# Kernel tuning notes

Measured on AMD Instinct MI355X. Metric: run time of the kernel, lower is better.

Reference implementation:

```python
import jax, jax.numpy as jnp
import numpy as np

T = 32768
H = 1024
N_HARM = 100
N_NOISE = 65
N_MLP = 3
LN_EPS = 1e-6

def exp_sigmoid(x, exponent=10.0, max_value=2.0, threshold=1e-7):
    return max_value * jax.nn.sigmoid(x) ** jnp.log(exponent) + threshold

def setup_inputs() -> dict:
    key = jax.random.key(0)
    ks = jax.random.split(key, 16)
    g = lambda k, shape, fan_in: jax.random.normal(k, shape, jnp.float32) / np.sqrt(fan_in)
    return {
        "f0": jax.random.uniform(ks[0], (T,), jnp.float32),
        "loudness": jax.random.normal(ks[1], (T,), jnp.float32),
        "W_in": g(ks[2], (2, H), 2), "b_in": jnp.zeros((H,), jnp.float32),
        "Wi": g(ks[3], (H, 3 * H), H),      # input kernels [r|z|n], no bias
        "Wh": g(ks[4], (H, 3 * H), H),      # hidden kernels [r|z|n]
        "b_h": jnp.zeros((3 * H,), jnp.float32),
        "h0": jnp.zeros((H,), jnp.float32),
        "mlp_W": g(ks[5], (N_MLP, H, H), H), "mlp_b": jnp.zeros((N_MLP, H), jnp.float32),
        "ln_scale": jnp.ones((N_MLP, H), jnp.float32), "ln_bias": jnp.zeros((N_MLP, H), jnp.float32),
        "amp_W": g(ks[6], (H, 1), H), "amp_b": jnp.zeros((1,), jnp.float32),
        "harm_W": g(ks[7], (H, N_HARM), H), "harm_b": jnp.zeros((N_HARM,), jnp.float32),
        "noise_W": g(ks[8], (H, N_NOISE), H), "noise_b": jnp.full((N_NOISE,), -5.0, jnp.float32),
    }

def _layernorm(x, scale, bias):
    mu = jnp.mean(x, axis=-1, keepdims=True)
    var = jnp.mean(jnp.square(x - mu), axis=-1, keepdims=True)
    return (x - mu) * jax.lax.rsqrt(var + LN_EPS) * scale + bias

def reference(f0, loudness, W_in, b_in, Wi, Wh, b_h, h0, mlp_W, mlp_b, ln_scale, ln_bias,
              amp_W, amp_b, harm_W, harm_b, noise_W, noise_b):
    features = jnp.stack([f0, loudness], axis=-1)          # [T, 2]
    projected = features @ W_in + b_in                     # [T, H]
    # Precompute input-side gate projections for all timesteps (one big GEMM).
    gi_all = projected @ Wi                                # [T, 3H]

    def gru_step(h, gi):
        gh = h @ Wh + b_h                                  # [3H]
        gi_r, gi_z, gi_n = jnp.split(gi, 3)
        gh_r, gh_z, gh_n = jnp.split(gh, 3)
        r = jax.nn.sigmoid(gi_r + gh_r)
        z = jax.nn.sigmoid(gi_z + gh_z)
        n = jnp.tanh(gi_n + r * gh_n)
        h_new = (1.0 - z) * n + z * h
        return h_new, h_new

    _, h = jax.lax.scan(gru_step, h0, gi_all)              # [T, H]
    for i in range(N_MLP):
        h = jax.nn.relu(_layernorm(h @ mlp_W[i] + mlp_b[i], ln_scale[i], ln_bias[i]))
    overall_amp = exp_sigmoid(h @ amp_W + amp_b)           # [T, 1]
    harmonic_dist = exp_sigmoid(h @ harm_W + harm_b)       # [T, N_HARM]
    noise_mags = h @ noise_W + noise_b                     # [T, N_NOISE]
    harmonic_dist = harmonic_dist / (jnp.sum(harmonic_dist, axis=-1, keepdims=True) + 1e-8)
    amplitudes = overall_amp * harmonic_dist
    return (amplitudes, noise_mags)
```

## Files before the change

kernel.cpp:

```cpp
#include <hip/hip_runtime.h>
#include <cstdint>
#include <cmath>


#define T_STEPS 32768
#define H_DIM   1024
#define H3      3072
#define NHARM   100
#define NNOISE  65
#define GRU_NB  64
#define GRU_THR 512
#define GRU_CPB 16

#define SLOT_SET_U32 2048

typedef unsigned short u16;
typedef unsigned uv4 __attribute__((ext_vector_type(4)));
typedef unsigned uv2 __attribute__((ext_vector_type(2)));

__device__ __forceinline__ float b2f(u16 u) {
  union { unsigned u; float f; } x; x.u = ((unsigned)u) << 16; return x.f;
}
__device__ __forceinline__ u16 f2b(float f) {
  unsigned v = __float_as_uint(f);
  unsigned r = (v + 0x7FFFu + ((v >> 16) & 1u)) >> 16;
  return (u16)r;
}
__device__ __forceinline__ float sigm(float x) { return 1.0f / (1.0f + expf(-x)); }
__device__ __forceinline__ float exp_sig(float x) {
  float s = sigm(x);
  return 2.0f * expf(2.302585093f * logf(s)) + 1e-7f;
}

__device__ __forceinline__ void poll_load_1(const unsigned* p, uv4& a) {
  asm volatile("global_load_dwordx4 %0, %1, off sc1\n\t"
               "s_waitcnt vmcnt(0)"
               : "=v"(a) : "v"(p) : "memory");
}
__device__ __forceinline__ void publish_x2(unsigned* p, unsigned t, float h) {
  uv2 v; v.x = t; v.y = __float_as_uint(h);
  asm volatile("global_store_dwordx2 %0, %1, off sc1"
               :: "v"(p), "v"(v) : "memory");
}

__global__ __launch_bounds__(256) void ddsp_precompute(
    const float* __restrict__ Win, const float* __restrict__ bin,
    const float* __restrict__ Wi, const float* __restrict__ h0,
    float* __restrict__ U, float* __restrict__ V, float* __restrict__ Wc,
    unsigned* __restrict__ slots)
{
  const int gid = blockIdx.x * 256 + threadIdx.x;
  if (blockIdx.x < 12) {
    const int j = gid;
    float su = 0.f, sv = 0.f, sw = 0.f;
    for (int h = 0; h < H_DIM; ++h) {
      const float wv = Wi[h * H3 + j];
      su = fmaf(Win[h], wv, su);
      sv = fmaf(Win[H_DIM + h], wv, sv);
      sw = fmaf(bin[h], wv, sw);
    }
    U[j] = su; V[j] = sv; Wc[j] = sw;
  } else {
    const int idx = gid - 12 * 256;
    unsigned* p0 = slots + (size_t)idx * 2;
    unsigned* p1 = slots + SLOT_SET_U32 + (size_t)idx * 2;
    p0[0] = 0u;
    p0[1] = __float_as_uint(h0[idx]);
    p1[0] = 0u;
    p1[1] = 0u;
  }
}

__device__ __forceinline__ void stage_gate(
    float4 (&dst)[8], const float* __restrict__ Wh, float* wg_lds,
    int g, int tid, int i, int jl, int bx)
{
  __syncthreads();
  for (int pass = 0; pass < 32; ++pass) {
    const int k = pass * 32 + (tid >> 4);
    const int c = tid & 15;
    wg_lds[c * H_DIM + k] = Wh[(size_t)k * H3 + g * H_DIM + bx * GRU_CPB + c];
  }
  __syncthreads();
  const int kbase = i << 5;
#pragma unroll
  for (int it = 0; it < 8; ++it) {
    const int kk = kbase + (((it + i) & 7) << 2);
    dst[it] = *(const float4*)(wg_lds + jl * H_DIM + kk);
  }
}

__global__ __launch_bounds__(512, 1) void ddsp_gru(
    const float* __restrict__ f0, const float* __restrict__ loud,
    const float* __restrict__ Wh, const float* __restrict__ bh,
    const float* __restrict__ U, const float* __restrict__ V,
    const float* __restrict__ Wc,
    unsigned* __restrict__ slots, u16* __restrict__ hall)
{
  __shared__ float wg_lds[GRU_CPB * H_DIM];
  __shared__ float lds_h[2][H_DIM];
  __shared__ float lds_hout[GRU_CPB];
  const int tid = threadIdx.x;
  const int i  = tid & 31;
  const int jl = tid >> 5;
  const int jg = blockIdx.x * GRU_CPB + jl;

  float ur = 0.f, uz = 0.f, un = 0.f, vr = 0.f, vz = 0.f, vn = 0.f;
  float wr = 0.f, wz = 0.f, wn = 0.f, bhr = 0.f, bhz = 0.f, bhn = 0.f;
  if (i == 0) {
    ur = U[jg]; uz = U[jg + 1024]; un = U[jg + 2048];
    vr = V[jg]; vz = V[jg + 1024]; vn = V[jg + 2048];
    wr = Wc[jg]; wz = Wc[jg + 1024]; wn = Wc[jg + 2048];
    bhr = bh[jg]; bhz = bh[jg + 1024]; bhn = bh[jg + 2048];
  }

  float4 wr4[8], wz4[8], wn4[8];
  stage_gate(wr4, Wh, wg_lds, 0, tid, i, jl, blockIdx.x);
  stage_gate(wz4, Wh, wg_lds, 1, tid, i, jl, blockIdx.x);
  stage_gate(wn4, Wh, wg_lds, 2, tid, i, jl, blockIdx.x);

  const int kbase = i << 5;

  for (int t = 0; t < T_STEPS; ++t) {
    const unsigned tag = (unsigned)t;
    const int par = t & 1;
    const unsigned* slot_rd = slots + (size_t)par * SLOT_SET_U32;
    unsigned*       slot_wr = slots + (size_t)(par ^ 1) * SLOT_SET_U32;

    const float fv = f0[t];
    const float lv = loud[t];

    {
      const unsigned* p = slot_rd + (size_t)tid * 4;
      uv4 a;
      do {
        poll_load_1(p, a);
      } while (a.x != tag || a.z != tag);
      float2 hq;
      hq.x = __uint_as_float(a.y); hq.y = __uint_as_float(a.w);
      *(float2*)(&lds_h[par][tid * 2]) = hq;
    }
    __syncthreads();

    const float hp = lds_h[par][jg];

    float a0 = 0.f, a1 = 0.f, a2 = 0.f;
#pragma unroll
    for (int it = 0; it < 8; ++it) {
      const int kk = kbase + (((it + i) & 7) << 2);
      const float4 h4 = *(const float4*)(&lds_h[par][kk]);
      a0 = fmaf(wr4[it].x, h4.x, a0); a0 = fmaf(wr4[it].y, h4.y, a0);
      a0 = fmaf(wr4[it].z, h4.z, a0); a0 = fmaf(wr4[it].w, h4.w, a0);
      a1 = fmaf(wz4[it].x, h4.x, a1); a1 = fmaf(wz4[it].y, h4.y, a1);
      a1 = fmaf(wz4[it].z, h4.z, a1); a1 = fmaf(wz4[it].w, h4.w, a1);
      a2 = fmaf(wn4[it].x, h4.x, a2); a2 = fmaf(wn4[it].y, h4.y, a2);
      a2 = fmaf(wn4[it].z, h4.z, a2); a2 = fmaf(wn4[it].w, h4.w, a2);
    }
#pragma unroll
    for (int m = 1; m < 32; m <<= 1) {
      a0 += __shfl_xor(a0, m);
      a1 += __shfl_xor(a1, m);
      a2 += __shfl_xor(a2, m);
    }
    float hn = 0.f;
    if (i == 0) {
      const float gir = fmaf(fv, ur, fmaf(lv, vr, wr));
      const float giz = fmaf(fv, uz, fmaf(lv, vz, wz));
      const float gin = fmaf(fv, un, fmaf(lv, vn, wn));
      const float r = sigm(gir + a0 + bhr);
      const float z = sigm(giz + a1 + bhz);
      const float n = tanhf(fmaf(r, a2 + bhn, gin));
      hn = (1.0f - z) * n + z * hp;
      lds_hout[jl] = hn;
    }
    __syncthreads();

    if (tid < GRU_CPB) {
      publish_x2(slot_wr + (size_t)(blockIdx.x * GRU_CPB + tid) * 2,
                 (unsigned)(t + 1), lds_hout[tid]);
    }
    if (i == 0) {
      hall[(size_t)t * H_DIM + jg] = f2b(hn);
    }
  }
}

__global__ __launch_bounds__(256) void ddsp_gemm_bias(
    const u16* __restrict__ X, const float* __restrict__ Wt,
    const float* __restrict__ bias, u16* __restrict__ Y)
{
  __shared__ float As[16][64];
  __shared__ float Bs[16][64];
  const int tid = threadIdx.x;
  const int R0 = blockIdx.x * 64;
  const int N0 = blockIdx.y * 64;
  const int tx = tid & 15, ty = tid >> 4;
  const int am = tid >> 2, ak = (tid & 3) * 4;
  const int bk = tid >> 4, bn = (tid & 15) * 4;
  float acc[4][4] = {};

  for (int k0 = 0; k0 < H_DIM; k0 += 16) {
    const ushort4 a4 = *(const ushort4*)(X + (size_t)(R0 + am) * H_DIM + k0 + ak);
    const float4 b4 = *(const float4*)(Wt + (size_t)(k0 + bk) * H_DIM + N0 + bn);
    As[ak + 0][am] = b2f(a4.x); As[ak + 1][am] = b2f(a4.y);
    As[ak + 2][am] = b2f(a4.z); As[ak + 3][am] = b2f(a4.w);
    *(float4*)&Bs[bk][bn] = b4;
    __syncthreads();
#pragma unroll
    for (int kk = 0; kk < 16; ++kk) {
      const float4 av = *(const float4*)&As[kk][ty * 4];
      const float4 bv = *(const float4*)&Bs[kk][tx * 4];
      const float a[4] = {av.x, av.y, av.z, av.w};
      const float b[4] = {bv.x, bv.y, bv.z, bv.w};
#pragma unroll
      for (int mi = 0; mi < 4; ++mi)
#pragma unroll
        for (int ni = 0; ni < 4; ++ni)
          acc[mi][ni] = fmaf(a[mi], b[ni], acc[mi][ni]);
    }
    __syncthreads();
  }
  const float4 bv4 = *(const float4*)(bias + N0 + tx * 4);
#pragma unroll
  for (int mi = 0; mi < 4; ++mi) {
    ushort4 st;
    st.x = f2b(acc[mi][0] + bv4.x);
    st.y = f2b(acc[mi][1] + bv4.y);
    st.z = f2b(acc[mi][2] + bv4.z);
    st.w = f2b(acc[mi][3] + bv4.w);
    *(ushort4*)(Y + (size_t)(R0 + ty * 4 + mi) * H_DIM + N0 + tx * 4) = st;
  }
}

__global__ __launch_bounds__(256) void ddsp_ln_relu(
    u16* __restrict__ Y, const float* __restrict__ scale, const float* __restrict__ bias)
{
  __shared__ float wsum[4], wsq[4];
  const int row = blockIdx.x, tid = threadIdx.x;
  const ushort4 r4 = *(const ushort4*)(Y + (size_t)row * H_DIM + tid * 4);
  float x[4] = {b2f(r4.x), b2f(r4.y), b2f(r4.z), b2f(r4.w)};
  float s = x[0] + x[1] + x[2] + x[3];
  float q = x[0] * x[0] + x[1] * x[1] + x[2] * x[2] + x[3] * x[3];
#pragma unroll
  for (int off = 32; off >= 1; off >>= 1) {
    s += __shfl_down(s, off);
    q += __shfl_down(q, off);
  }
  if ((tid & 63) == 0) { wsum[tid >> 6] = s; wsq[tid >> 6] = q; }
  __syncthreads();
  const float ts = wsum[0] + wsum[1] + wsum[2] + wsum[3];
  const float tq = wsq[0] + wsq[1] + wsq[2] + wsq[3];
  const float mu = ts * (1.0f / H_DIM);
  const float var = tq * (1.0f / H_DIM) - mu * mu;
  const float rstd = rsqrtf(fmaxf(var, 0.f) + 1e-6f);
  const float4 sc = *(const float4*)(scale + tid * 4);
  const float4 bi = *(const float4*)(bias + tid * 4);
  ushort4 st;
  st.x = f2b(fmaxf((x[0] - mu) * rstd * sc.x + bi.x, 0.f));
  st.y = f2b(fmaxf((x[1] - mu) * rstd * sc.y + bi.y, 0.f));
  st.z = f2b(fmaxf((x[2] - mu) * rstd * sc.z + bi.z, 0.f));
  st.w = f2b(fmaxf((x[3] - mu) * rstd * sc.w + bi.w, 0.f));
  *(ushort4*)(Y + (size_t)row * H_DIM + tid * 4) = st;
}

__global__ __launch_bounds__(256) void ddsp_heads(
    const u16* __restrict__ Hf,
    const float* __restrict__ aW, const float* __restrict__ ab,
    const float* __restrict__ hW, const float* __restrict__ hb,
    const float* __restrict__ nW, const float* __restrict__ nb,
    float* __restrict__ out)
{
  __shared__ float lh[H_DIM];
  __shared__ float se[128];
  __shared__ float sred[2];
  const int t = blockIdx.x, tid = threadIdx.x;
  const ushort4 h4 = *(const ushort4*)(Hf + (size_t)t * H_DIM + tid * 4);
  lh[tid * 4 + 0] = b2f(h4.x); lh[tid * 4 + 1] = b2f(h4.y);
  lh[tid * 4 + 2] = b2f(h4.z); lh[tid * 4 + 3] = b2f(h4.w);
  __syncthreads();

  if (tid < NHARM) {
    float acc = 0.f;
    for (int k = 0; k < H_DIM; k += 4) {
      const float4 hv = *(const float4*)(lh + k);
      acc = fmaf(hv.x, hW[(k + 0) * NHARM + tid], acc);
      acc = fmaf(hv.y, hW[(k + 1) * NHARM + tid], acc);
      acc = fmaf(hv.z, hW[(k + 2) * NHARM + tid], acc);
      acc = fmaf(hv.w, hW[(k + 3) * NHARM + tid], acc);
    }
    se[tid] = exp_sig(acc + hb[tid]);
  } else if (tid < NHARM + NNOISE) {
    const int n = tid - NHARM;
    float acc = 0.f;
    for (int k = 0; k < H_DIM; k += 4) {
      const float4 hv = *(const float4*)(lh + k);
      acc = fmaf(hv.x, nW[(k + 0) * NNOISE + n], acc);
      acc = fmaf(hv.y, nW[(k + 1) * NNOISE + n], acc);
      acc = fmaf(hv.z, nW[(k + 2) * NNOISE + n], acc);
      acc = fmaf(hv.w, nW[(k + 3) * NNOISE + n], acc);
    }
    out[(size_t)T_STEPS * NHARM + (size_t)t * NNOISE + n] = acc + nb[n];
  } else if (tid == NHARM + NNOISE) {
    float acc = 0.f;
    for (int k = 0; k < H_DIM; k += 4) {
      const float4 hv = *(const float4*)(lh + k);
      acc = fmaf(hv.x, aW[k + 0], acc);
      acc = fmaf(hv.y, aW[k + 1], acc);
      acc = fmaf(hv.z, aW[k + 2], acc);
      acc = fmaf(hv.w, aW[k + 3], acc);
    }
    sred[0] = exp_sig(acc + ab[0]);
  }
  if (tid >= NHARM && tid < 128) se[tid] = 0.f;
  __syncthreads();
  if (tid < 64) {
    float s2 = se[tid] + se[tid + 64];
#pragma unroll
    for (int off = 32; off >= 1; off >>= 1) s2 += __shfl_down(s2, off);
    if (tid == 0) sred[1] = s2;
  }
  __syncthreads();
  if (tid < NHARM) {
    out[(size_t)t * NHARM + tid] = sred[0] * se[tid] / (sred[1] + 1e-8f);
  }
}

extern "C" void kernel_launch(void* const* d_in, const int* in_sizes, int n_in,
                              void* d_out, int out_size, void* d_ws, size_t ws_size,
                              hipStream_t stream)
{
  (void)in_sizes; (void)n_in; (void)out_size;
  const float* f0   = (const float*)d_in[0];
  const float* loud = (const float*)d_in[1];
  const float* Win  = (const float*)d_in[2];
  const float* bin  = (const float*)d_in[3];
  const float* Wi   = (const float*)d_in[4];
  const float* Wh   = (const float*)d_in[5];
  const float* bh   = (const float*)d_in[6];
  const float* h0   = (const float*)d_in[7];
  const float* mlpW = (const float*)d_in[8];
  const float* mlpb = (const float*)d_in[9];
  const float* lnS  = (const float*)d_in[10];
  const float* lnB  = (const float*)d_in[11];
  const float* aW   = (const float*)d_in[12];
  const float* ab   = (const float*)d_in[13];
  const float* hW   = (const float*)d_in[14];
  const float* hb   = (const float*)d_in[15];
  const float* nW   = (const float*)d_in[16];
  const float* nb   = (const float*)d_in[17];
  float* out = (float*)d_out;

  char* ws = (char*)d_ws;
  float*    U     = (float*)(ws);
  float*    V     = (float*)(ws + 12288);
  float*    Wc    = (float*)(ws + 24576);
  u16* bufA = (u16*)(ws + 53248);
  u16* bufB = (u16*)(ws + 53248 + (size_t)T_STEPS * H_DIM * 2);
  unsigned* slots = (unsigned*)bufB;

  const size_t needed = 53248 + 2 * (size_t)T_STEPS * H_DIM * 2;
  if (ws_size < needed) {
    return;
  }

  ddsp_precompute<<<16, 256, 0, stream>>>(Win, bin, Wi, h0, U, V, Wc, slots);
  ddsp_gru<<<GRU_NB, GRU_THR, 0, stream>>>(f0, loud, Wh, bh, U, V, Wc, slots, bufA);

  dim3 gg(T_STEPS / 64, H_DIM / 64);
  ddsp_gemm_bias<<<gg, 256, 0, stream>>>(bufA, mlpW, mlpb, bufB);
  ddsp_ln_relu<<<T_STEPS, 256, 0, stream>>>(bufB, lnS, lnB);
  ddsp_gemm_bias<<<gg, 256, 0, stream>>>(bufB, mlpW + (size_t)H_DIM * H_DIM, mlpb + H_DIM, bufA);
  ddsp_ln_relu<<<T_STEPS, 256, 0, stream>>>(bufA, lnS + H_DIM, lnB + H_DIM);
  ddsp_gemm_bias<<<gg, 256, 0, stream>>>(bufA, mlpW + 2 * (size_t)H_DIM * H_DIM, mlpb + 2 * H_DIM, bufB);
  ddsp_ln_relu<<<T_STEPS, 256, 0, stream>>>(bufB, lnS + 2 * H_DIM, lnB + 2 * H_DIM);

  ddsp_heads<<<T_STEPS, 256, 0, stream>>>(bufB, aW, ab, hW, hb, nW, nb, out);
}
```

Baseline: 71.27 ms.

## Pipeline spin-poll loads and compute gate outputs in one wave

The spin-wait on the hidden-state exchange slots now keeps two loads in flight, waiting with vmcnt(1) instead of vmcnt(0), to shorten the poll round-trip on the serial GRU critical path. The gate nonlinearities are also moved so that lanes 0-15 of the first wave compute all 16 columns from partial sums written to LDS, then publish and store directly. This removes the separate hout staging step but keeps a barrier before the epilogue. It adds extra memory traffic from redundant polls and concentrates the transcendental work on one wave.

```diff
diff --git a/kernel.cpp b/kernel.cpp
--- a/kernel.cpp
+++ b/kernel.cpp
@@ -32,10 +32,17 @@
   return 2.0f * expf(2.302585093f * logf(s)) + 1e-7f;
 }
 
-__device__ __forceinline__ void poll_load_1(const unsigned* p, uv4& a) {
-  asm volatile("global_load_dwordx4 %0, %1, off sc1\n\t"
-               "s_waitcnt vmcnt(0)"
+__device__ __forceinline__ void poll_issue1(const unsigned* p, uv4& a) {
+  asm volatile("global_load_dwordx4 %0, %1, off sc1"
                : "=v"(a) : "v"(p) : "memory");
+}
+__device__ __forceinline__ void wait_vm1() {
+  asm volatile("s_waitcnt vmcnt(1)" ::: "memory");
+  __builtin_amdgcn_sched_barrier(0);
+}
+__device__ __forceinline__ void wait_vm0() {
+  asm volatile("s_waitcnt vmcnt(0)" ::: "memory");
+  __builtin_amdgcn_sched_barrier(0);
 }
 __device__ __forceinline__ void publish_x2(unsigned* p, unsigned t, float h) {
   uv2 v; v.x = t; v.y = __float_as_uint(h);
@@ -99,19 +106,20 @@
 {
   __shared__ float wg_lds[GRU_CPB * H_DIM];
   __shared__ float lds_h[2][H_DIM];
-  __shared__ float lds_hout[GRU_CPB];
+  __shared__ float sums[GRU_CPB][4];
   const int tid = threadIdx.x;
   const int i  = tid & 31;
   const int jl = tid >> 5;
-  const int jg = blockIdx.x * GRU_CPB + jl;
+  const int jg0 = blockIdx.x * GRU_CPB;
 
   float ur = 0.f, uz = 0.f, un = 0.f, vr = 0.f, vz = 0.f, vn = 0.f;
   float wr = 0.f, wz = 0.f, wn = 0.f, bhr = 0.f, bhz = 0.f, bhn = 0.f;
-  if (i == 0) {
-    ur = U[jg]; uz = U[jg + 1024]; un = U[jg + 2048];
-    vr = V[jg]; vz = V[jg + 1024]; vn = V[jg + 2048];
-    wr = Wc[jg]; wz = Wc[jg + 1024]; wn = Wc[jg + 2048];
-    bhr = bh[jg]; bhz = bh[jg + 1024]; bhn = bh[jg + 2048];
+  if (tid < GRU_CPB) {
+    const int c = jg0 + tid;
+    ur = U[c]; uz = U[c + 1024]; un = U[c + 2048];
+    vr = V[c]; vz = V[c + 1024]; vn = V[c + 2048];
+    wr = Wc[c]; wz = Wc[c + 1024]; wn = Wc[c + 2048];
+    bhr = bh[c]; bhz = bh[c + 1024]; bhn = bh[c + 2048];
   }
 
   float4 wr4[8], wz4[8], wn4[8];
@@ -132,17 +140,28 @@
 
     {
       const unsigned* p = slot_rd + (size_t)tid * 4;
-      uv4 a;
-      do {
-        poll_load_1(p, a);
-      } while (a.x != tag || a.z != tag);
+      uv4 A, B;
       float2 hq;
-      hq.x = __uint_as_float(a.y); hq.y = __uint_as_float(a.w);
+      poll_issue1(p, A);
+      poll_issue1(p, B);
+      for (;;) {
+        wait_vm1();
+        if (A.x == tag && A.z == tag) {
+          hq.x = __uint_as_float(A.y); hq.y = __uint_as_float(A.w);
+          break;
+        }
+        poll_issue1(p, A);
+        wait_vm1();
+        if (B.x == tag && B.z == tag) {
+          hq.x = __uint_as_float(B.y); hq.y = __uint_as_float(B.w);
+          break;
+        }
+        poll_issue1(p, B);
+      }
+      wait_vm0();
       *(float2*)(&lds_h[par][tid * 2]) = hq;
     }
     __syncthreads();
-
-    const float hp = lds_h[par][jg];
 
     float a0 = 0.f, a1 = 0.f, a2 = 0.f;
 #pragma unroll
@@ -162,25 +181,23 @@
       a1 += __shfl_xor(a1, m);
       a2 += __shfl_xor(a2, m);
     }
-    float hn = 0.f;
-    if (i == 0) {
+    if (i < 3) sums[jl][i] = (i == 0) ? a0 : ((i == 1) ? a1 : a2);
+    __syncthreads();
+
+    if (tid < GRU_CPB) {
+      const float s0 = sums[tid][0];
+      const float s1 = sums[tid][1];
+      const float s2 = sums[tid][2];
       const float gir = fmaf(fv, ur, fmaf(lv, vr, wr));
       const float giz = fmaf(fv, uz, fmaf(lv, vz, wz));
       const float gin = fmaf(fv, un, fmaf(lv, vn, wn));
-      const float r = sigm(gir + a0 + bhr);
-      const float z = sigm(giz + a1 + bhz);
-      const float n = tanhf(fmaf(r, a2 + bhn, gin));
-      hn = (1.0f - z) * n + z * hp;
-      lds_hout[jl] = hn;
-    }
-    __syncthreads();
-
-    if (tid < GRU_CPB) {
-      publish_x2(slot_wr + (size_t)(blockIdx.x * GRU_CPB + tid) * 2,
-                 (unsigned)(t + 1), lds_hout[tid]);
-    }
-    if (i == 0) {
-      hall[(size_t)t * H_DIM + jg] = f2b(hn);
+      const float r = sigm(gir + s0 + bhr);
+      const float z = sigm(giz + s1 + bhz);
+      const float n = tanhf(fmaf(r, s2 + bhn, gin));
+      const float hp = lds_h[par][jg0 + tid];
+      const float hn = (1.0f - z) * n + z * hp;
+      publish_x2(slot_wr + (size_t)(jg0 + tid) * 2, (unsigned)(t + 1), hn);
+      hall[(size_t)t * H_DIM + jg0 + tid] = f2b(hn);
     }
   }
 }
```

New measurement: 79.01 ms. 10.9% more time.
